# Kernel optimization log

Measured on AMD Instinct MI355X. Metric: run time of the kernel, lower is better.

Reference implementation:

```python
import jax, jax.numpy as jnp
import numpy as np

EPS1 = 1e-8
EPS2 = 1e-5
H_BW = 1.0  # bandwidth h
MSE_W = 1.0
CTX_W = 1.0
PERC_W = 0.02


def _contextual_similarity(out_feat, tgt_feat):
    """Batched contextual similarity (Mechrez et al. 2018).

    out_feat, tgt_feat: [B, C, Hf, Wf]. Returns scalar (mean over batch).
    Matches the torch loop-over-samples / loop-over-target-vectors math,
    fully vectorized as one batched pairwise-cosine + softmax + max.
    """
    B, C = out_feat.shape[0], out_feat.shape[1]
    # X, Y: [B, N, C] with N = Hf*Wf spatial positions
    X = out_feat.reshape(B, C, -1).transpose(0, 2, 1)
    Y = tgt_feat.reshape(B, C, -1).transpose(0, 2, 1)
    X = X - X.mean(axis=1, keepdims=True)  # center per channel over positions
    Y = Y - Y.mean(axis=1, keepdims=True)
    xn = jnp.linalg.norm(X, axis=2)  # [B, N]
    yn = jnp.linalg.norm(Y, axis=2)  # [B, N]
    # cosine distance d[b, x, y] = 1 - <X_x, Y_y> / (|X_x||Y_y| + eps1)
    S = jnp.einsum('bxc,byc->bxy', X, Y)
    d = 1.0 - S / (xn[:, :, None] * yn[:, None, :] + EPS1)
    # normalize by min over target vectors y (torch: dxy.min(dim=0) with dxy [Ny, Nx])
    d_ = d / (d.min(axis=2, keepdims=True) + EPS2)
    w = jnp.exp((1.0 - d_) / H_BW)
    c = w / w.sum(axis=2, keepdims=True)  # softmax over y per x
    # torch: cxy.max(dim=1)[0].mean() -> max over x for each y, mean over y
    CS = c.max(axis=1).mean(axis=1)  # [B]
    return CS.mean()


def _mse(a, b):
    return jnp.mean((a - b) ** 2)


def setup_inputs() -> dict:
    key = jax.random.key(0)
    k1, k2, k3, k4 = jax.random.split(key, 4)
    outputs = jax.random.normal(k1, (4, 3, 256, 256), dtype=jnp.float32)
    targets = jax.random.normal(k2, (4, 3, 256, 256), dtype=jnp.float32)
    output_features = jax.random.normal(k3, (4, 256, 64, 64), dtype=jnp.float32)
    target_features = jax.random.normal(k4, (4, 256, 64, 64), dtype=jnp.float32)
    return {"outputs": outputs, "targets": targets,
            "output_features": output_features, "target_features": target_features}


def reference(outputs, targets, output_features, target_features):
    loss = MSE_W * _mse(outputs, targets)
    loss = loss - CTX_W * jnp.log(_contextual_similarity(output_features, target_features))
    loss = loss + PERC_W * _mse(output_features, target_features)
    return loss
```

## Files before the change

### kernel.cpp

```cpp
#include <hip/hip_runtime.h>
#include <hip/hip_bf16.h>
#include <cstdint>

#define EPS2f 1e-5f

typedef __bf16 bf16x8 __attribute__((ext_vector_type(8)));
typedef float floatx4 __attribute__((ext_vector_type(4)));
typedef _Float16 half8 __attribute__((ext_vector_type(8)));
typedef __fp16 fp16x2 __attribute__((ext_vector_type(2)));

static constexpr int Bn = 4, Cn = 256, Nn = 4096;

static constexpr size_t MSE1P = 0;
static constexpr size_t MSE2P = 256;
static constexpr size_t CSP   = 1536;
static constexpr size_t MEANX = 2560;
static constexpr size_t MEANY = 3584;
static constexpr size_t IXN   = 4608;
static constexpr size_t IYN   = 20992;
static constexpr size_t DMIN  = 37376;
static constexpr size_t RSUM  = 53760;
static constexpr size_t XCO   = 70144;
static constexpr size_t YCO   = 70144 + 2097152;
static constexpr size_t SOFF  = 70144 + 2 * 2097152;

__device__ __forceinline__ unsigned short f2bf(float f) {
    unsigned u = __float_as_uint(f);
    u += 0x7fffu + ((u >> 16) & 1u);
    return (unsigned short)(u >> 16);
}

__global__ __launch_bounds__(256) void prep1(const float4* __restrict__ outs,
                                             const float4* __restrict__ tgts,
                                             const float4* __restrict__ of4,
                                             const float4* __restrict__ tf4,
                                             float* __restrict__ ws) {
    const int bid = blockIdx.x, t = threadIdx.x;
    __shared__ float red[12];
    if (bid < 1024) {
        const int c = bid & 255, b = bid >> 8;
        const float4* po = of4 + ((size_t)b * Cn + c) * (Nn / 4);
        const float4* pt = tf4 + ((size_t)b * Cn + c) * (Nn / 4);
        float so = 0.f, st = 0.f, sq = 0.f;
        for (int i = t; i < 1024; i += 256) {
            float4 o = po[i], q = pt[i];
            so += o.x + o.y + o.z + o.w;
            st += q.x + q.y + q.z + q.w;
            float dx = o.x - q.x, dy = o.y - q.y, dz = o.z - q.z, dw = o.w - q.w;
            sq += dx * dx + dy * dy + dz * dz + dw * dw;
        }
        for (int m = 1; m < 64; m <<= 1) {
            so += __shfl_xor(so, m); st += __shfl_xor(st, m); sq += __shfl_xor(sq, m);
        }
        if ((t & 63) == 0) { int w = t >> 6; red[w * 3] = so; red[w * 3 + 1] = st; red[w * 3 + 2] = sq; }
        __syncthreads();
        if (t == 0) {
            so = red[0] + red[3] + red[6] + red[9];
            st = red[1] + red[4] + red[7] + red[10];
            sq = red[2] + red[5] + red[8] + red[11];
            ws[MEANX + b * Cn + c] = so * (1.f / 4096.f);
            ws[MEANY + b * Cn + c] = st * (1.f / 4096.f);
            ws[MSE2P + bid] = sq;
        }
    } else if (bid < 1216) {
        const int base = bid - 1024;
        float sq = 0.f;
        for (int i = base * 256 + t; i < 196608; i += 192 * 256) {
            float4 a = outs[i], b4 = tgts[i];
            float dx = a.x - b4.x, dy = a.y - b4.y, dz = a.z - b4.z, dw = a.w - b4.w;
            sq += dx * dx + dy * dy + dz * dz + dw * dw;
        }
        for (int m = 1; m < 64; m <<= 1) sq += __shfl_xor(sq, m);
        if ((t & 63) == 0) red[t >> 6] = sq;
        __syncthreads();
        if (t == 0) ws[MSE1P + base] = red[0] + red[1] + red[2] + red[3];
    } else {
        const int i = (bid - 1216) * 256 + t;
        ws[DMIN + i] = (i < 16384) ? __builtin_inff() : 0.f;
    }
}

__global__ __launch_bounds__(256) void center_fused(const float* __restrict__ ofeat,
                                                    const float* __restrict__ tfeat,
                                                    float* __restrict__ ws) {
    const int b = blockIdx.y, nb = blockIdx.x, z = blockIdx.z;
    const float* feat = z ? tfeat : ofeat;
    const float* mean = ws + (z ? MEANY : MEANX);
    unsigned short* outb = (unsigned short*)(ws + (z ? YCO : XCO));
    float* inv = ws + (z ? IYN : IXN);
    __shared__ float mean_s[256];
    __shared__ float sq_s[256];
    const int t = threadIdx.x;
    mean_s[t] = mean[b * Cn + t];
    __syncthreads();
    const int pos = t & 63, cg = t >> 6;
    const int n = nb * 64 + pos;
    const float* fb = feat + (size_t)b * Cn * Nn;
    unsigned short* ob = outb + ((size_t)b * Nn + n) * Cn;
    float ss = 0.f;
    for (int c0 = cg * 64; c0 < cg * 64 + 64; c0 += 8) {
        unsigned short tmp[8];
        #pragma unroll
        for (int u = 0; u < 8; ++u) {
            float v = fb[(size_t)(c0 + u) * Nn + n] - mean_s[c0 + u];
            ss += v * v;
            tmp[u] = f2bf(v);
        }
        uint4 pk;
        pk.x = (unsigned)tmp[0] | ((unsigned)tmp[1] << 16);
        pk.y = (unsigned)tmp[2] | ((unsigned)tmp[3] << 16);
        pk.z = (unsigned)tmp[4] | ((unsigned)tmp[5] << 16);
        pk.w = (unsigned)tmp[6] | ((unsigned)tmp[7] << 16);
        *(uint4*)(ob + c0) = pk;
    }
    sq_s[t] = ss;
    __syncthreads();
    if (t < 64) {
        float s = sq_s[t] + sq_s[t + 64] + sq_s[t + 128] + sq_s[t + 192];
        inv[(size_t)b * Nn + nb * 64 + t] = 1.f / sqrtf(s);
    }
}

__global__ __launch_bounds__(256) void gemm_store(const unsigned short* __restrict__ Xc,
                                                  const unsigned short* __restrict__ Yc,
                                                  const float* __restrict__ ixn,
                                                  const float* __restrict__ iyn,
                                                  float* __restrict__ dmin,
                                                  _Float16* __restrict__ S) {
    __shared__ __align__(16) unsigned short smem[16384];
    __shared__ float ixn_s[128], iyn_s[128];

    const int t = threadIdx.x;
    const int bx = blockIdx.x, by = blockIdx.y, b = blockIdx.z;
    const size_t nb = (size_t)b * Nn;

    if (t < 128) ixn_s[t] = ixn[nb + bx * 128 + t];
    else iyn_s[t - 128] = iyn[nb + by * 128 + (t - 128)];

    const int wid = t >> 6, lane = t & 63;
    const int wm = wid >> 1, wn = wid & 1;
    const int lr = lane & 15, lq = lane >> 4;
    const int srow = t >> 2, sq = t & 3;

    const unsigned short* Ag = Xc + (nb + bx * 128) * Cn;
    const unsigned short* Bg = Yc + (nb + by * 128) * Cn;
    const unsigned short* Ga0 = Ag + (size_t)srow * Cn + sq * 8;
    const unsigned short* Ga1 = Ag + (size_t)(srow + 64) * Cn + sq * 8;
    const unsigned short* Gb0 = Bg + (size_t)srow * Cn + sq * 8;
    const unsigned short* Gb1 = Bg + (size_t)(srow + 64) * Cn + sq * 8;
    const int wA0 = (sq * 128 + srow) * 8;
    const int wA1 = (sq * 128 + srow + 64) * 8;

    floatx4 acc[4][4];
    #pragma unroll
    for (int i = 0; i < 4; i++)
        #pragma unroll
        for (int j = 0; j < 4; j++) acc[i][j] = (floatx4){0.f, 0.f, 0.f, 0.f};

    {
        uint4 a0 = *(const uint4*)Ga0, a1 = *(const uint4*)Ga1;
        uint4 b0 = *(const uint4*)Gb0, b1 = *(const uint4*)Gb1;
        *(uint4*)(smem + wA0) = a0;
        *(uint4*)(smem + wA1) = a1;
        *(uint4*)(smem + 4096 + wA0) = b0;
        *(uint4*)(smem + 4096 + wA1) = b1;
    }
    __syncthreads();

    #pragma unroll
    for (int ks = 0; ks < 8; ks++) {
        const int cur = (ks & 1) * 8192, nxt = 8192 - cur;
        uint4 a0, a1, b0, b1;
        if (ks < 7) {
            a0 = *(const uint4*)(Ga0 + (ks + 1) * 32);
            a1 = *(const uint4*)(Ga1 + (ks + 1) * 32);
            b0 = *(const uint4*)(Gb0 + (ks + 1) * 32);
            b1 = *(const uint4*)(Gb1 + (ks + 1) * 32);
        }
        bf16x8 af[4], bv[4];
        #pragma unroll
        for (int i = 0; i < 4; i++)
            af[i] = *(const bf16x8*)(smem + cur + (lq * 128 + wm * 64 + i * 16 + lr) * 8);
        #pragma unroll
        for (int j = 0; j < 4; j++)
            bv[j] = *(const bf16x8*)(smem + cur + 4096 + (lq * 128 + wn * 64 + j * 16 + lr) * 8);
        #pragma unroll
        for (int i = 0; i < 4; i++)
            #pragma unroll
            for (int j = 0; j < 4; j++)
                acc[i][j] = __builtin_amdgcn_mfma_f32_16x16x32_bf16(af[i], bv[j], acc[i][j], 0, 0, 0);
        if (ks < 7) {
            *(uint4*)(smem + nxt + wA0) = a0;
            *(uint4*)(smem + nxt + wA1) = a1;
            *(uint4*)(smem + nxt + 4096 + wA0) = b0;
            *(uint4*)(smem + nxt + 4096 + wA1) = b1;
            __syncthreads();
        }
    }

    float ix[16];
    #pragma unroll
    for (int i = 0; i < 4; i++)
        #pragma unroll
        for (int r = 0; r < 4; r++) ix[i * 4 + r] = ixn_s[wm * 64 + i * 16 + lq * 4 + r];
    float rmin[16];
    #pragma unroll
    for (int k = 0; k < 16; k++) rmin[k] = __builtin_inff();
    #pragma unroll
    for (int i = 0; i < 4; i++)
        #pragma unroll
        for (int j = 0; j < 4; j++) {
            const float iy = iyn_s[wn * 64 + j * 16 + lr];
            #pragma unroll
            for (int r = 0; r < 4; r++)
                rmin[i * 4 + r] = fminf(rmin[i * 4 + r], 1.f - acc[i][j][r] * ix[i * 4 + r] * iy);
        }
    #pragma unroll
    for (int m = 1; m < 16; m <<= 1)
        #pragma unroll
        for (int k = 0; k < 16; k++) rmin[k] = fminf(rmin[k], __shfl_xor(rmin[k], m));
    if (lr == 0) {
        #pragma unroll
        for (int i = 0; i < 4; i++)
            #pragma unroll
            for (int r = 0; r < 4; r++)
                atomicMin((int*)&dmin[nb + bx * 128 + wm * 64 + i * 16 + lq * 4 + r],
                          __float_as_int(rmin[i * 4 + r]));
    }
    __syncthreads();

    #pragma unroll
    for (int i = 0; i < 4; i++) {
        const int xlocal = wm * 64 + i * 16 + lq * 4;
        #pragma unroll
        for (int j = 0; j < 4; j++) {
            const int ylocal = wn * 64 + j * 16 + lr;
            const float iy = iyn_s[ylocal];
            float c0 = acc[i][j][0] * ix[i * 4 + 0] * iy;
            float c1 = acc[i][j][1] * ix[i * 4 + 1] * iy;
            float c2 = acc[i][j][2] * ix[i * 4 + 2] * iy;
            float c3 = acc[i][j][3] * ix[i * 4 + 3] * iy;
            fp16x2 p0 = __builtin_amdgcn_cvt_pkrtz(c0, c1);
            fp16x2 p1 = __builtin_amdgcn_cvt_pkrtz(c2, c3);
            *(float2*)(smem + ylocal * 128 + (xlocal ^ ((ylocal & 15) * 8))) =
                make_float2(__builtin_bit_cast(float, p0), __builtin_bit_cast(float, p1));
        }
    }
    __syncthreads();

    #pragma unroll
    for (int p = 0; p < 8; p++) {
        const int yl = wid * 32 + p * 4 + (lane >> 4);
        const int ch = lane & 15;
        uint4 v = *(const uint4*)(smem + yl * 128 + ((ch * 8) ^ ((yl & 15) * 8)));
        *(uint4*)(S + (nb + by * 128 + yl) * (size_t)Nn + bx * 128 + ch * 8) = v;
    }
}

__global__ __launch_bounds__(256) void b1_rsum(const _Float16* __restrict__ S,
                                               const float* __restrict__ dmin,
                                               float* __restrict__ rsum) {
    __shared__ float red[32 * 65];
    const int t = threadIdx.x;
    const int x0 = blockIdx.x * 64, ys = blockIdx.y, b = blockIdx.z;
    const int chunk = t & 7, yg = t >> 3;
    const int xbase = x0 + chunk * 8;
    const size_t gb = (size_t)b * Nn;

    float invd[8], av[8];
    #pragma unroll
    for (int u = 0; u < 8; u++) {
        float dm = dmin[gb + xbase + u];
        invd[u] = 1.f / (dm + EPS2f);
        av[u] = 1.f - invd[u];
    }
    float s[8];
    #pragma unroll
    for (int u = 0; u < 8; u++) s[u] = 0.f;

    for (int k = 0; k < 16; k++) {
        const int y = ys * 512 + yg + 32 * k;
        half8 hv = *(const half8*)(S + (gb + y) * Nn + xbase);
        #pragma unroll
        for (int u = 0; u < 8; u++)
            s[u] += __expf(fmaf((float)hv[u], invd[u], av[u]));
    }
    #pragma unroll
    for (int u = 0; u < 8; u++) red[yg * 65 + chunk * 8 + u] = s[u];
    __syncthreads();
    if (t < 64) {
        float rs = 0.f;
        #pragma unroll 8
        for (int g = 0; g < 32; g++) rs += red[g * 65 + t];
        atomicAdd(&rsum[gb + x0 + t], rs);
    }
}

__global__ __launch_bounds__(256) void b2_cmax(const _Float16* __restrict__ S,
                                               const float* __restrict__ dmin,
                                               const float* __restrict__ rsum,
                                               float* __restrict__ csp) {
    __shared__ float ps[512 * 20];
    __shared__ float red2[16];
    const int t = threadIdx.x, b = blockIdx.y;
    const size_t gb = (size_t)b * Nn;
    for (int i = t; i < Nn; i += 256) {
        float iv = 1.f / (dmin[gb + i] + EPS2f);
        float gg = 1.f - iv - __logf(rsum[gb + i]);
        int c = i >> 3, e = i & 7;
        ps[c * 20 + e * 2] = iv;
        ps[c * 20 + e * 2 + 1] = gg;
    }
    __syncthreads();

    const int lanegrp = t & 15, yloc = t >> 4;
    const int y = blockIdx.x * 16 + yloc;
    const _Float16* Sy = S + (gb + y) * Nn;

    float cm = 0.f;
    for (int k = 0; k < 32; k++) {
        const int chunk = lanegrp + 16 * k;
        half8 hv = *(const half8*)(Sy + chunk * 8);
        const float* pp = &ps[chunk * 20];
        float4 p01 = *(const float4*)(pp);
        float4 p23 = *(const float4*)(pp + 4);
        float4 p45 = *(const float4*)(pp + 8);
        float4 p67 = *(const float4*)(pp + 12);
        float iv[8] = {p01.x, p01.z, p23.x, p23.z, p45.x, p45.z, p67.x, p67.z};
        float gg[8] = {p01.y, p01.w, p23.y, p23.w, p45.y, p45.w, p67.y, p67.w};
        #pragma unroll
        for (int u = 0; u < 8; u++)
            cm = fmaxf(cm, __expf(fmaf((float)hv[u], iv[u], gg[u])));
    }
    #pragma unroll
    for (int m = 1; m < 16; m <<= 1) cm = fmaxf(cm, __shfl_xor(cm, m));
    if (lanegrp == 0) red2[yloc] = cm;
    __syncthreads();
    if (t == 0) {
        float s2 = 0.f;
        #pragma unroll
        for (int i = 0; i < 16; i++) s2 += red2[i];
        csp[b * 256 + blockIdx.x] = s2;
    }
}

__global__ __launch_bounds__(256) void finalize_kernel(const float* __restrict__ ws,
                                                       float* __restrict__ out) {
    const int t = threadIdx.x;
    float s1 = 0.f, s2 = 0.f, s3 = 0.f;
    if (t < 192) s1 = ws[MSE1P + t];
    for (int i = t; i < 1024; i += 256) { s2 += ws[MSE2P + i]; s3 += ws[CSP + i]; }
    for (int m = 1; m < 64; m <<= 1) {
        s1 += __shfl_xor(s1, m); s2 += __shfl_xor(s2, m); s3 += __shfl_xor(s3, m);
    }
    __shared__ float red[12];
    if ((t & 63) == 0) { int w = t >> 6; red[w * 3] = s1; red[w * 3 + 1] = s2; red[w * 3 + 2] = s3; }
    __syncthreads();
    if (t == 0) {
        s1 = red[0] + red[3] + red[6] + red[9];
        s2 = red[1] + red[4] + red[7] + red[10];
        s3 = red[2] + red[5] + red[8] + red[11];
        float cs = s3 * (1.f / 16384.f);
        out[0] = s1 * (1.f / 786432.f) - logf(cs) + 0.02f * s2 * (1.f / 4194304.f);
    }
}

extern "C" void kernel_launch(void* const* d_in, const int* in_sizes, int n_in,
                              void* d_out, int out_size, void* d_ws, size_t ws_size,
                              hipStream_t stream) {
    const float* outputs = (const float*)d_in[0];
    const float* targets = (const float*)d_in[1];
    const float* ofeat   = (const float*)d_in[2];
    const float* tfeat   = (const float*)d_in[3];
    float* ws  = (float*)d_ws;
    float* out = (float*)d_out;

    unsigned short* Xc = (unsigned short*)(ws + XCO);
    unsigned short* Yc = (unsigned short*)(ws + YCO);
    _Float16* S = (_Float16*)(ws + SOFF);

    prep1<<<1344, 256, 0, stream>>>((const float4*)outputs, (const float4*)targets,
                                    (const float4*)ofeat, (const float4*)tfeat, ws);
    center_fused<<<dim3(Nn / 64, Bn, 2), 256, 0, stream>>>(ofeat, tfeat, ws);
    gemm_store<<<dim3(Nn / 128, Nn / 128, Bn), 256, 0, stream>>>(Xc, Yc, ws + IXN, ws + IYN,
                                                                 ws + DMIN, S);
    b1_rsum<<<dim3(64, 8, Bn), 256, 0, stream>>>(S, ws + DMIN, ws + RSUM);
    b2_cmax<<<dim3(Nn / 16, Bn), 256, 0, stream>>>(S, ws + DMIN, ws + RSUM, ws + CSP);
    finalize_kernel<<<1, 256, 0, stream>>>(ws, out);
}
```

Baseline: 237.9 us.

## Stage GEMM tiles via direct global-to-LDS loads and remap blocks per XCD

The bf16 GEMM now copies its operand tiles straight from global memory into LDS with global_load_lds 16-byte transfers. This replaces the register round-trip and the separate LDS stores. The LDS tile layout changes from k-chunk-major to row-major 32-element rows, and the fragment reads are rewritten to match. The launch also becomes a flat grid, with block indices remapped so each XCD works on one batch and one half of the columns, aiming for better L2 reuse of operand tiles. The risks are new LDS bank conflicts from the 64-byte row stride and relying on correct waitcnt handling before the barrier.

```diff
diff --git a/kernel.cpp b/kernel.cpp
--- a/kernel.cpp
+++ b/kernel.cpp
@@ -28,6 +28,12 @@
     unsigned u = __float_as_uint(f);
     u += 0x7fffu + ((u >> 16) & 1u);
     return (unsigned short)(u >> 16);
+}
+
+__device__ __forceinline__ void stage16(const unsigned short* g, unsigned short* l) {
+    __builtin_amdgcn_global_load_lds(
+        (const __attribute__((address_space(1))) unsigned int*)g,
+        (__attribute__((address_space(3))) unsigned int*)l, 16, 0, 0);
 }
 
 __global__ __launch_bounds__(256) void prep1(const float4* __restrict__ outs,
@@ -131,7 +137,11 @@
     __shared__ float ixn_s[128], iyn_s[128];
 
     const int t = threadIdx.x;
-    const int bx = blockIdx.x, by = blockIdx.y, b = blockIdx.z;
+    const int lin = blockIdx.x;
+    const int xcd = lin & 7, idx = lin >> 3;
+    const int b = xcd >> 1;
+    const int by = (xcd & 1) * 16 + (idx & 15);
+    const int bx = idx >> 4;
     const size_t nb = (size_t)b * Nn;
 
     if (t < 128) ixn_s[t] = ixn[nb + bx * 128 + t];
@@ -140,16 +150,13 @@
     const int wid = t >> 6, lane = t & 63;
     const int wm = wid >> 1, wn = wid & 1;
     const int lr = lane & 15, lq = lane >> 4;
-    const int srow = t >> 2, sq = t & 3;
 
     const unsigned short* Ag = Xc + (nb + bx * 128) * Cn;
-    const unsigned short* Bg = Yc + (nb + by * 128) * Cn;
-    const unsigned short* Ga0 = Ag + (size_t)srow * Cn + sq * 8;
-    const unsigned short* Ga1 = Ag + (size_t)(srow + 64) * Cn + sq * 8;
-    const unsigned short* Gb0 = Bg + (size_t)srow * Cn + sq * 8;
-    const unsigned short* Gb1 = Bg + (size_t)(srow + 64) * Cn + sq * 8;
-    const int wA0 = (sq * 128 + srow) * 8;
-    const int wA1 = (sq * 128 + srow + 64) * 8;
+    const unsigned short* Bg =Yc + (nb + by * 128) * Cn;
+    const int lrow = lane >> 2, lsl = (lane & 3) * 8;
+    const unsigned short* gA = Ag + (size_t)(wid * 32 + lrow) * Cn + lsl;
+    const unsigned short* gB = Bg + (size_t)(wid * 32 + lrow) * Cn + lsl;
+    const int w1024 = wid * 1024;
 
     floatx4 acc[4][4];
     #pragma unroll
@@ -157,45 +164,35 @@
         #pragma unroll
         for (int j = 0; j < 4; j++) acc[i][j] = (floatx4){0.f, 0.f, 0.f, 0.f};
 
-    {
-        uint4 a0 = *(const uint4*)Ga0, a1 = *(const uint4*)Ga1;
-        uint4 b0 = *(const uint4*)Gb0, b1 = *(const uint4*)Gb1;
-        *(uint4*)(smem + wA0) = a0;
-        *(uint4*)(smem + wA1) = a1;
-        *(uint4*)(smem + 4096 + wA0) = b0;
-        *(uint4*)(smem + 4096 + wA1) = b1;
-    }
+    stage16(gA, smem + w1024);
+    stage16(gA + 16 * Cn, smem + w1024 + 512);
+    stage16(gB, smem + 4096 + w1024);
+    stage16(gB + 16 * Cn, smem + 4096 + w1024 + 512);
     __syncthreads();
 
     #pragma unroll
     for (int ks = 0; ks < 8; ks++) {
         const int cur = (ks & 1) * 8192, nxt = 8192 - cur;
-        uint4 a0, a1, b0, b1;
         if (ks < 7) {
-            a0 = *(const uint4*)(Ga0 + (ks + 1) * 32);
-            a1 = *(const uint4*)(Ga1 + (ks + 1) * 32);
-            b0 = *(const uint4*)(Gb0 + (ks + 1) * 32);
-            b1 = *(const uint4*)(Gb1 + (ks + 1) * 32);
+            const int koff = (ks + 1) * 32;
+            stage16(gA + koff, smem + nxt + w1024);
+            stage16(gA + koff + 16 * Cn, smem + nxt + w1024 + 512);
+            stage16(gB + koff, smem + nxt + 4096 + w1024);
+            stage16(gB + koff + 16 * Cn, smem + nxt + 4096 + w1024 + 512);
         }
         bf16x8 af[4], bv[4];
         #pragma unroll
         for (int i = 0; i < 4; i++)
-            af[i] = *(const bf16x8*)(smem + cur + (lq * 128 + wm * 64 + i * 16 + lr) * 8);
+            af[i] = *(const bf16x8*)(smem + cur + (wm * 64 + i * 16 + lr) * 32 + lq * 8);
         #pragma unroll
         for (int j = 0; j < 4; j++)
-            bv[j] = *(const bf16x8*)(smem + cur + 4096 + (lq * 128 + wn * 64 + j * 16 + lr) * 8);
+            bv[j] = *(const bf16x8*)(smem + cur + 4096 + (wn * 64 + j * 16 + lr) * 32 + lq * 8);
         #pragma unroll
         for (int i = 0; i < 4; i++)
             #pragma unroll
             for (int j = 0; j < 4; j++)
                 acc[i][j] = __builtin_amdgcn_mfma_f32_16x16x32_bf16(af[i], bv[j], acc[i][j], 0, 0, 0);
-        if (ks < 7) {
-            *(uint4*)(smem + nxt + wA0) = a0;
-            *(uint4*)(smem + nxt + wA1) = a1;
-            *(uint4*)(smem + nxt + 4096 + wA0) = b0;
-            *(uint4*)(smem + nxt + 4096 + wA1) = b1;
-            __syncthreads();
-        }
+        if (ks < 7) __syncthreads();
     }
 
     float ix[16];
@@ -382,8 +379,7 @@
     prep1<<<1344, 256, 0, stream>>>((const float4*)outputs, (const float4*)targets,
                                     (const float4*)ofeat, (const float4*)tfeat, ws);
     center_fused<<<dim3(Nn / 64, Bn, 2), 256, 0, stream>>>(ofeat, tfeat, ws);
-    gemm_store<<<dim3(Nn / 128, Nn / 128, Bn), 256, 0, stream>>>(Xc, Yc, ws + IXN, ws + IYN,
-                                                                 ws + DMIN, S);
+    gemm_store<<<4096, 256, 0, stream>>>(Xc, Yc, ws + IXN, ws + IYN, ws + DMIN, S);
     b1_rsum<<<dim3(64, 8, Bn), 256, 0, stream>>>(S, ws + DMIN, ws + RSUM);
     b2_cmax<<<dim3(Nn / 16, Bn), 256, 0, stream>>>(S, ws + DMIN, ws + RSUM, ws + CSP);
     finalize_kernel<<<1, 256, 0, stream>>>(ws, out);
```

Measured after the change: 257.2 us. +8.1%, slower.
